# Kernel optimization log

Measured on AMD Instinct MI355X. Metric: run time of the kernel, lower is better.

Reference implementation:

```python
import jax, jax.numpy as jnp
import numpy as np

N, K, G = 4096, 4096, 128  # out_features, in_features, groupsize


def setup_inputs() -> dict:
    key = jax.random.key(0)
    k1, k2, k3, k4 = jax.random.split(key, 4)
    input = jax.random.normal(k1, (1, 2048, K), dtype=jnp.float32)
    # packed int4 weights: each byte holds two 4-bit codes (high nibble = even k, low = odd k)
    weight_packed = jax.random.randint(k2, (N, K // 2), 0, 256, dtype=jnp.int32)
    scales = jax.random.uniform(k3, (K // G, N), dtype=jnp.float32) * 0.02 + 1e-3
    zeros = jax.random.normal(k4, (K // G, N), dtype=jnp.float32) * 0.05
    scales_and_zeros = jnp.stack([scales, zeros], axis=-1)  # (K//G, N, 2)
    return {"input": input, "weight_packed": weight_packed,
            "scales_and_zeros": scales_and_zeros, "groupsize": G}


def reference(input, weight_packed, scales_and_zeros, groupsize):
    n, k_half = weight_packed.shape
    k = 2 * k_half
    g = k // groupsize
    # unpack two int4 codes per byte: high nibble first (even k index), then low nibble
    hi = (weight_packed >> 4) & 0xF
    lo = weight_packed & 0xF
    q = jnp.stack([hi, lo], axis=-1).reshape(n, k)  # (N, K), codes in [0,15]
    scales = scales_and_zeros[..., 0].T  # (N, G)
    zeros = scales_and_zeros[..., 1].T   # (N, G)
    # group-wise affine dequant: w = (q - 8) * scale + zero
    qg = q.reshape(n, g, groupsize).astype(jnp.float32)
    w = (qg - 8.0) * scales[:, :, None] + zeros[:, :, None]  # (N, G, gs)
    w = w.reshape(n, k)
    # out[..., n] = sum_k input[..., k] * w[n, k]
    return jnp.einsum('bsk,nk->bsn', input, w)
```

## Files before the change

kernel.cpp:

```cpp
#include <hip/hip_runtime.h>
#include <hip/hip_bf16.h>


using bf16x8 = __attribute__((ext_vector_type(8))) short;
using f32x4  = __attribute__((ext_vector_type(4))) float;

#define KK 4096
#define NN 4096
#define NT (KK / 64)

static __device__ __forceinline__ short f2bf(float f) {
    __hip_bfloat16 h = __float2bfloat16(f);
    return __builtin_bit_cast(short, h);
}

#define GLDS16(gptr, lptr) __builtin_amdgcn_global_load_lds( \
    (const __attribute__((address_space(1))) void*)(gptr),   \
    (__attribute__((address_space(3))) void*)(lptr), 16, 0, 0)

#define MFMA16 __builtin_amdgcn_mfma_f32_16x16x32_bf16

__global__ __launch_bounds__(256) void dequant_w(
    const int* __restrict__ W, const float* __restrict__ SZ,
    short* __restrict__ Wd)
{
    const int idx = blockIdx.x * 256 + threadIdx.x;
    const int n   = idx >> 9;
    const int q4  = idx & 511;
    const int kh0 = q4 << 2;
    const int g   = kh0 >> 6;
    const float2 sz = *(const float2*)(SZ + ((size_t)g * NN + n) * 2);
    const float scale = sz.x;
    const float zs    = sz.y - 8.0f * sz.x;
    int4 p = *(const int4*)(W + (size_t)n * (KK / 2) + kh0);
    int vals[4] = {p.x, p.y, p.z, p.w};
    bf16x8 r;
    #pragma unroll
    for (int j = 0; j < 4; ++j) {
        int v = vals[j];
        r[2 * j]     = f2bf((float)((v >> 4) & 0xF) * scale + zs);
        r[2 * j + 1] = f2bf((float)(v & 0xF) * scale + zs);
    }
    *(bf16x8*)&Wd[(size_t)n * KK + (kh0 << 1)] = r;
}

__global__ __launch_bounds__(256) void cvt_a(
    const float* __restrict__ A, short* __restrict__ Ab)
{
    const int idx = blockIdx.x * 256 + threadIdx.x;
    const float4* s = (const float4*)(A + (size_t)idx * 8);
    float4 u = s[0], v = s[1];
    bf16x8 r;
    r[0] = f2bf(u.x); r[1] = f2bf(u.y); r[2] = f2bf(u.z); r[3] = f2bf(u.w);
    r[4] = f2bf(v.x); r[5] = f2bf(v.y); r[6] = f2bf(v.z); r[7] = f2bf(v.w);
    *(bf16x8*)&Ab[(size_t)idx * 8] = r;
}

__global__ __launch_bounds__(512, 2) void gemm_8ph(
    const short* __restrict__ Ab, const short* __restrict__ Bb,
    float* __restrict__ C)
{
    __shared__ short sA[3 * 256 * 64];
    __shared__ short sB[3 * 128 * 64];

    const int tid  = threadIdx.x;
    const int lane = tid & 63;
    const int wave = tid >> 6;
    const int wm   = wave >> 1;
    const int wn   = wave & 1;
    const int bm   = blockIdx.y * 256;
    const int bn   = blockIdx.x * 128;

    const int sl = lane >> 3;
    const int sc = (lane & 7) ^ sl;
    const short* aSt = Ab + (size_t)(bm + wave * 32 + sl) * KK + sc * 8;
    const short* bSt = Bb + (size_t)(bn + wave * 16 + sl) * KK + sc * 8;

    const int l15 = lane & 15;
    const int pc0 = (((lane >> 4)) ^ (lane & 7)) * 8;
    const int pc1 = ((4 | (lane >> 4)) ^ (lane & 7)) * 8;
    const int aRd = wm * 4096 + l15 * 64;
    const int bRd = wn * 4096 + l15 * 64;

    f32x4 acc[4][4] = {};
    bf16x8 aF[2][2], bF[2][2][2];

    #pragma unroll
    for (int l = 0; l < 4; ++l)
        GLDS16(aSt + l * 8 * KK,      &sA[(wave * 32 + l * 8) * 64]);
    #pragma unroll
    for (int l = 0; l < 2; ++l)
        GLDS16(bSt + l * 8 * KK,      &sB[(wave * 16 + l * 8) * 64]);
    #pragma unroll
    for (int l = 0; l < 4; ++l)
        GLDS16(aSt + l * 8 * KK + 64, &sA[16384 + (wave * 32 + l * 8) * 64]);
    #pragma unroll
    for (int l = 0; l < 2; ++l)
        GLDS16(bSt + l * 8 * KK + 64, &sB[8192 + (wave * 16 + l * 8) * 64]);
    asm volatile("s_waitcnt vmcnt(6)" ::: "memory");
    __builtin_amdgcn_s_barrier();

    int cur = 0;
    for (int t = 0; t < NT; ++t) {
        const int nxt = (cur == 0) ? 2 : cur - 1;
        const short* sAc = &sA[cur * 16384];
        const short* sBc = &sB[cur * 8192];
        short* sAn = &sA[nxt * 16384];
        short* sBn = &sB[nxt * 8192];
        const bool st = (t + 2 < NT);
        const int gk = (t + 2) * 64;

        aF[0][0] = *(const bf16x8*)&sAc[aRd + pc0];
        aF[0][1] = *(const bf16x8*)&sAc[aRd + pc1];
        aF[1][0] = *(const bf16x8*)&sAc[aRd + 1024 + pc0];
        aF[1][1] = *(const bf16x8*)&sAc[aRd + 1024 + pc1];
        bF[0][0][0] = *(const bf16x8*)&sBc[bRd + pc0];
        bF[0][0][1] = *(const bf16x8*)&sBc[bRd + pc1];
        bF[0][1][0] = *(const bf16x8*)&sBc[bRd + 1024 + pc0];
        bF[0][1][1] = *(const bf16x8*)&sBc[bRd + 1024 + pc1];
        if (st) {
            GLDS16(aSt + 0 * 8 * KK + gk, sAn + (wave * 32 + 0) * 64);
            GLDS16(aSt + 1 * 8 * KK + gk, sAn + (wave * 32 + 8) * 64);
        }
        __builtin_amdgcn_s_barrier();
        asm volatile("s_waitcnt lgkmcnt(0)" ::: "memory");
        __builtin_amdgcn_s_setprio(1);
        acc[0][0] = MFMA16(aF[0][0], bF[0][0][0], acc[0][0], 0, 0, 0);
        acc[0][0] = MFMA16(aF[0][1], bF[0][0][1], acc[0][0], 0, 0, 0);
        acc[0][1] = MFMA16(aF[0][0], bF[0][1][0], acc[0][1], 0, 0, 0);
        acc[0][1] = MFMA16(aF[0][1], bF[0][1][1], acc[0][1], 0, 0, 0);
        acc[1][0] = MFMA16(aF[1][0], bF[0][0][0], acc[1][0], 0, 0, 0);
        acc[1][0] = MFMA16(aF[1][1], bF[0][0][1], acc[1][0], 0, 0, 0);
        acc[1][1] = MFMA16(aF[1][0], bF[0][1][0], acc[1][1], 0, 0, 0);
        acc[1][1] = MFMA16(aF[1][1], bF[0][1][1], acc[1][1], 0, 0, 0);
        __builtin_amdgcn_s_setprio(0);
        __builtin_amdgcn_s_barrier();

        bF[1][0][0] = *(const bf16x8*)&sBc[bRd + 2048 + pc0];
        bF[1][0][1] = *(const bf16x8*)&sBc[bRd + 2048 + pc1];
        bF[1][1][0] = *(const bf16x8*)&sBc[bRd + 3072 + pc0];
        bF[1][1][1] = *(const bf16x8*)&sBc[bRd + 3072 + pc1];
        if (st) {
            GLDS16(aSt + 2 * 8 * KK + gk, sAn + (wave * 32 + 16) * 64);
            GLDS16(aSt + 3 * 8 * KK + gk, sAn + (wave * 32 + 24) * 64);
        }
        __builtin_amdgcn_s_barrier();
        asm volatile("s_waitcnt lgkmcnt(0)" ::: "memory");
        __builtin_amdgcn_s_setprio(1);
        acc[0][2] = MFMA16(aF[0][0], bF[1][0][0], acc[0][2], 0, 0, 0);
        acc[0][2] = MFMA16(aF[0][1], bF[1][0][1], acc[0][2], 0, 0, 0);
        acc[0][3] = MFMA16(aF[0][0], bF[1][1][0], acc[0][3], 0, 0, 0);
        acc[0][3] = MFMA16(aF[0][1], bF[1][1][1], acc[0][3], 0, 0, 0);
        acc[1][2] = MFMA16(aF[1][0], bF[1][0][0], acc[1][2], 0, 0, 0);
        acc[1][2] = MFMA16(aF[1][1], bF[1][0][1], acc[1][2], 0, 0, 0);
        acc[1][3] = MFMA16(aF[1][0], bF[1][1][0], acc[1][3], 0, 0, 0);
        acc[1][3] = MFMA16(aF[1][1], bF[1][1][1], acc[1][3], 0, 0, 0);
        __builtin_amdgcn_s_setprio(0);
        __builtin_amdgcn_s_barrier();

        aF[0][0] = *(const bf16x8*)&sAc[aRd + 2048 + pc0];
        aF[0][1] = *(const bf16x8*)&sAc[aRd + 2048 + pc1];
        aF[1][0] = *(const bf16x8*)&sAc[aRd + 3072 + pc0];
        aF[1][1] = *(const bf16x8*)&sAc[aRd + 3072 + pc1];
        if (st) {
            GLDS16(bSt + 0 * 8 * KK + gk, sBn + (wave * 16 + 0) * 64);
            GLDS16(bSt + 1 * 8 * KK + gk, sBn + (wave * 16 + 8) * 64);
        }
        __builtin_amdgcn_s_barrier();
        asm volatile("s_waitcnt lgkmcnt(0)" ::: "memory");
        __builtin_amdgcn_s_setprio(1);
        acc[2][2] = MFMA16(aF[0][0], bF[1][0][0], acc[2][2], 0, 0, 0);
        acc[2][2] = MFMA16(aF[0][1], bF[1][0][1], acc[2][2], 0, 0, 0);
        acc[2][3] = MFMA16(aF[0][0], bF[1][1][0], acc[2][3], 0, 0, 0);
        acc[2][3] = MFMA16(aF[0][1], bF[1][1][1], acc[2][3], 0, 0, 0);
        acc[3][2] = MFMA16(aF[1][0], bF[1][0][0], acc[3][2], 0, 0, 0);
        acc[3][2] = MFMA16(aF[1][1], bF[1][0][1], acc[3][2], 0, 0, 0);
        acc[3][3] = MFMA16(aF[1][0], bF[1][1][0], acc[3][3], 0, 0, 0);
        acc[3][3] = MFMA16(aF[1][1], bF[1][1][1], acc[3][3], 0, 0, 0);
        __builtin_amdgcn_s_setprio(0);
        __builtin_amdgcn_s_barrier();

        __builtin_amdgcn_s_setprio(1);
        acc[2][0] = MFMA16(aF[0][0], bF[0][0][0], acc[2][0], 0, 0, 0);
        acc[2][0] = MFMA16(aF[0][1], bF[0][0][1], acc[2][0], 0, 0, 0);
        acc[2][1] = MFMA16(aF[0][0], bF[0][1][0], acc[2][1], 0, 0, 0);
        acc[2][1] = MFMA16(aF[0][1], bF[0][1][1], acc[2][1], 0, 0, 0);
        acc[3][0] = MFMA16(aF[1][0], bF[0][0][0], acc[3][0], 0, 0, 0);
        acc[3][0] = MFMA16(aF[1][1], bF[0][0][1], acc[3][0], 0, 0, 0);
        acc[3][1] = MFMA16(aF[1][0], bF[0][1][0], acc[3][1], 0, 0, 0);
        acc[3][1] = MFMA16(aF[1][1], bF[0][1][1], acc[3][1], 0, 0, 0);
        __builtin_amdgcn_s_setprio(0);
        if (t < NT - 2) {
            asm volatile("s_waitcnt vmcnt(6)" ::: "memory");
        } else {
            asm volatile("s_waitcnt vmcnt(0)" ::: "memory");
        }
        __builtin_amdgcn_s_barrier();

        cur = (cur == 2) ? 0 : cur + 1;
    }

    float* Cp = C + (size_t)(bm + wm * 64) * NN + bn + wn * 64;
    const int cr = (lane >> 4) << 2;
    #pragma unroll
    for (int m = 0; m < 4; ++m) {
        #pragma unroll
        for (int j = 0; j < 4; ++j) {
            float* dst = Cp + (size_t)(m * 16 + cr + j) * NN + l15;
            #pragma unroll
            for (int n = 0; n < 4; ++n)
                dst[n * 16] = acc[m][n][j];
        }
    }
}

#define LDKF 72
__global__ __launch_bounds__(256) void wq4_gemm_fused(
    const float* __restrict__ A, const int* __restrict__ W,
    const float* __restrict__ SZ, float* __restrict__ C, int M)
{
    __shared__ short sA[128 * LDKF];
    __shared__ short sB[128 * LDKF];
    const int tid = threadIdx.x, lane = tid & 63, wave = tid >> 6;
    const int wr = (wave >> 1) << 6, wc = (wave & 1) << 6;
    const int bm = blockIdx.y * 128, bn = blockIdx.x * 128;
    const int ar = tid >> 2, ac = (tid & 3) << 4;
    const int br = tid >> 1, bh = (tid & 1) << 4;
    const float* Arow0 = A + (size_t)(bm + ar) * KK + ac;
    const float* Arow1 = A + (size_t)(bm + 64 + ar) * KK + ac;
    const int*   Wrow  = W + (size_t)(bn + br) * (KK / 2) + bh;
    const float* SZrow = SZ + (size_t)(bn + br) * 2;
    f32x4 acc[4][4] = {};
    for (int k0 = 0; k0 < KK; k0 += 64) {
        {
            const float4* s0 = (const float4*)(Arow0 + k0);
            const float4* s1 = (const float4*)(Arow1 + k0);
            float4 a0 = s0[0], a1 = s0[1], a2 = s0[2], a3 = s0[3];
            float4 b0 = s1[0], b1 = s1[1], b2 = s1[2], b3 = s1[3];
            auto cvt8 = [](float4 u, float4 v) -> bf16x8 {
                bf16x8 r;
                r[0] = f2bf(u.x); r[1] = f2bf(u.y); r[2] = f2bf(u.z); r[3] = f2bf(u.w);
                r[4] = f2bf(v.x); r[5] = f2bf(v.y); r[6] = f2bf(v.z); r[7] = f2bf(v.w);
                return r;
            };
            *(bf16x8*)&sA[ar * LDKF + ac]            = cvt8(a0, a1);
            *(bf16x8*)&sA[ar * LDKF + ac + 8]        = cvt8(a2, a3);
            *(bf16x8*)&sA[(64 + ar) * LDKF + ac]     = cvt8(b0, b1);
            *(bf16x8*)&sA[(64 + ar) * LDKF + ac + 8] = cvt8(b2, b3);
        }
        {
            const int g = k0 >> 7;
            const float2 sz = *(const float2*)(SZrow + (size_t)g * NN * 2);
            const float scale = sz.x, zs = sz.y - 8.0f * sz.x;
            const int4* src = (const int4*)(Wrow + (k0 >> 1));
            #pragma unroll
            for (int i = 0; i < 4; ++i) {
                int4 p = src[i];
                int vals[4] = {p.x, p.y, p.z, p.w};
                bf16x8 r;
                #pragma unroll
                for (int j = 0; j < 4; ++j) {
                    int v = vals[j];
                    r[2 * j]     = f2bf((float)((v >> 4) & 0xF) * scale + zs);
                    r[2 * j + 1] = f2bf((float)(v & 0xF) * scale + zs);
                }
                *(bf16x8*)&sB[br * LDKF + (bh << 1) + (i << 3)] = r;
            }
        }
        __syncthreads();
        #pragma unroll
        for (int ks = 0; ks < 2; ++ks) {
            const int col = (ks << 5) + ((lane >> 4) << 3);
            bf16x8 af[4], bfr[4];
            #pragma unroll
            for (int m = 0; m < 4; ++m)
                af[m] = *(const bf16x8*)&sA[(wr + m * 16 + (lane & 15)) * LDKF + col];
            #pragma unroll
            for (int n = 0; n < 4; ++n)
                bfr[n] = *(const bf16x8*)&sB[(wc + n * 16 + (lane & 15)) * LDKF + col];
            #pragma unroll
            for (int m = 0; m < 4; ++m)
                #pragma unroll
                for (int n = 0; n < 4; ++n)
                    acc[m][n] = __builtin_amdgcn_mfma_f32_16x16x32_bf16(
                        af[m], bfr[n], acc[m][n], 0, 0, 0);
        }
        __syncthreads();
    }
    float* Cp = C + (size_t)(bm + wr) * NN + bn + wc;
    const int cr = (lane >> 4) << 2, cc = lane & 15;
    #pragma unroll
    for (int m = 0; m < 4; ++m)
        #pragma unroll
        for (int j = 0; j < 4; ++j) {
            float* dst = Cp + (size_t)(m * 16 + cr + j) * NN + cc;
            #pragma unroll
            for (int n = 0; n < 4; ++n) dst[n * 16] = acc[m][n][j];
        }
}

extern "C" void kernel_launch(void* const* d_in, const int* in_sizes, int n_in,
                              void* d_out, int out_size, void* d_ws, size_t ws_size,
                              hipStream_t stream) {
    const float* A  = (const float*)d_in[0];
    const int*   W  = (const int*)d_in[1];
    const float* SZ = (const float*)d_in[2];
    float* C = (float*)d_out;

    const int M = in_sizes[0] / KK;

    const size_t wd_elems = (size_t)NN * KK;
    const size_t ab_elems = (size_t)M * KK;
    const size_t need = (wd_elems + ab_elems) * sizeof(short);

    if (ws_size >= need && (M % 256) == 0) {
        short* Wd = (short*)d_ws;
        short* Ab = Wd + wd_elems;
        dequant_w<<<NN * (KK / 8) / 256, 256, 0, stream>>>(W, SZ, Wd);
        cvt_a<<<(int)(ab_elems / 8 / 256), 256, 0, stream>>>(A, Ab);
        dim3 grid(NN / 128, M / 256);
        gemm_8ph<<<grid, dim3(512), 0, stream>>>(Ab, Wd, C);
    } else {
        dim3 grid(NN / 128, M / 128);
        wq4_gemm_fused<<<grid, dim3(256), 0, stream>>>(A, W, SZ, C, M);
    }
}
```

Before: 102.4 us.

## Switch bf16 GEMM inner loop to 32x32x16 MFMA with two-phase schedule

Replaces the 16x16x32 MFMA tiling in the main GEMM with 32x32x16 MFMA instructions, so each wave now holds four 32x32 accumulators instead of sixteen 16x16 ones. The per-tile schedule drops from four barrier-separated phases to two, with LDS fragment reads and async global-to-LDS prefetches redistributed across them. The aim is fewer LDS reads per FLOP and less barrier overhead. The cost is a different LDS read swizzle pattern and epilogue mapping, which may change bank conflicts and latency hiding.

After: 102.7 us. About the same (+0.2%).

```diff
diff --git a/kernel.cpp b/kernel.cpp
--- a/kernel.cpp
+++ b/kernel.cpp
@@ -3,7 +3,7 @@
 
 
 using bf16x8 = __attribute__((ext_vector_type(8))) short;
-using f32x4  = __attribute__((ext_vector_type(4))) float;
+using f32x16 = __attribute__((ext_vector_type(16))) float;
 
 #define KK 4096
 #define NN 4096
@@ -18,7 +18,7 @@
     (const __attribute__((address_space(1))) void*)(gptr),   \
     (__attribute__((address_space(3))) void*)(lptr), 16, 0, 0)
 
-#define MFMA16 __builtin_amdgcn_mfma_f32_16x16x32_bf16
+#define MFMA32 __builtin_amdgcn_mfma_f32_32x32x16_bf16
 
 __global__ __launch_bounds__(256) void dequant_w(
     const int* __restrict__ W, const float* __restrict__ SZ,
@@ -56,7 +56,7 @@
     *(bf16x8*)&Ab[(size_t)idx * 8] = r;
 }
 
-__global__ __launch_bounds__(512, 2) void gemm_8ph(
+__global__ __launch_bounds__(512, 2) void gemm32(
     const short* __restrict__ Ab, const short* __restrict__ Bb,
     float* __restrict__ C)
 {
@@ -76,27 +76,30 @@
     const short* aSt = Ab + (size_t)(bm + wave * 32 + sl) * KK + sc * 8;
     const short* bSt = Bb + (size_t)(bn + wave * 16 + sl) * KK + sc * 8;
 
-    const int l15 = lane & 15;
-    const int pc0 = (((lane >> 4)) ^ (lane & 7)) * 8;
-    const int pc1 = ((4 | (lane >> 4)) ^ (lane & 7)) * 8;
-    const int aRd = wm * 4096 + l15 * 64;
-    const int bRd = wn * 4096 + l15 * 64;
-
-    f32x4 acc[4][4] = {};
-    bf16x8 aF[2][2], bF[2][2][2];
+    const int l31 = lane & 31;
+    const int lx  = lane >> 5;
+    const int l7  = lane & 7;
+    const int px0 = ((0 + lx) ^ l7) * 8;
+    const int px1 = ((2 + lx) ^ l7) * 8;
+    const int px2 = ((4 + lx) ^ l7) * 8;
+    const int px3 = ((6 + lx) ^ l7) * 8;
+    const int aRd = (wm * 64 + l31) * 64;
+    const int bRd = (wn * 64 + l31) * 64;
+
+    f32x16 acc00 = {}, acc01 = {}, acc10 = {}, acc11 = {};
 
     #pragma unroll
     for (int l = 0; l < 4; ++l)
-        GLDS16(aSt + l * 8 * KK,      &sA[(wave * 32 + l * 8) * 64]);
+        GLDS16(aSt + (size_t)l * 8 * KK,      &sA[(wave * 32 + l * 8) * 64]);
     #pragma unroll
     for (int l = 0; l < 2; ++l)
-        GLDS16(bSt + l * 8 * KK,      &sB[(wave * 16 + l * 8) * 64]);
+        GLDS16(bSt + (size_t)l * 8 * KK,      &sB[(wave * 16 + l * 8) * 64]);
     #pragma unroll
     for (int l = 0; l < 4; ++l)
-        GLDS16(aSt + l * 8 * KK + 64, &sA[16384 + (wave * 32 + l * 8) * 64]);
+        GLDS16(aSt + (size_t)l * 8 * KK + 64, &sA[16384 + (wave * 32 + l * 8) * 64]);
     #pragma unroll
     for (int l = 0; l < 2; ++l)
-        GLDS16(bSt + l * 8 * KK + 64, &sB[8192 + (wave * 16 + l * 8) * 64]);
+        GLDS16(bSt + (size_t)l * 8 * KK + 64, &sB[8192 + (wave * 16 + l * 8) * 64]);
     asm volatile("s_waitcnt vmcnt(6)" ::: "memory");
     __builtin_amdgcn_s_barrier();
 
@@ -110,110 +113,97 @@
         const bool st = (t + 2 < NT);
         const int gk = (t + 2) * 64;
 
-        aF[0][0] = *(const bf16x8*)&sAc[aRd + pc0];
-        aF[0][1] = *(const bf16x8*)&sAc[aRd + pc1];
-        aF[1][0] = *(const bf16x8*)&sAc[aRd + 1024 + pc0];
-        aF[1][1] = *(const bf16x8*)&sAc[aRd + 1024 + pc1];
-        bF[0][0][0] = *(const bf16x8*)&sBc[bRd + pc0];
-        bF[0][0][1] = *(const bf16x8*)&sBc[bRd + pc1];
-        bF[0][1][0] = *(const bf16x8*)&sBc[bRd + 1024 + pc0];
-        bF[0][1][1] = *(const bf16x8*)&sBc[bRd + 1024 + pc1];
-        if (st) {
-            GLDS16(aSt + 0 * 8 * KK + gk, sAn + (wave * 32 + 0) * 64);
-            GLDS16(aSt + 1 * 8 * KK + gk, sAn + (wave * 32 + 8) * 64);
-        }
-        __builtin_amdgcn_s_barrier();
-        asm volatile("s_waitcnt lgkmcnt(0)" ::: "memory");
-        __builtin_amdgcn_s_setprio(1);
-        acc[0][0] = MFMA16(aF[0][0], bF[0][0][0], acc[0][0], 0, 0, 0);
-        acc[0][0] = MFMA16(aF[0][1], bF[0][0][1], acc[0][0], 0, 0, 0);
-        acc[0][1] = MFMA16(aF[0][0], bF[0][1][0], acc[0][1], 0, 0, 0);
-        acc[0][1] = MFMA16(aF[0][1], bF[0][1][1], acc[0][1], 0, 0, 0);
-        acc[1][0] = MFMA16(aF[1][0], bF[0][0][0], acc[1][0], 0, 0, 0);
-        acc[1][0] = MFMA16(aF[1][1], bF[0][0][1], acc[1][0], 0, 0, 0);
-        acc[1][1] = MFMA16(aF[1][0], bF[0][1][0], acc[1][1], 0, 0, 0);
-        acc[1][1] = MFMA16(aF[1][1], bF[0][1][1], acc[1][1], 0, 0, 0);
-        __builtin_amdgcn_s_setprio(0);
-        __builtin_amdgcn_s_barrier();
-
-        bF[1][0][0] = *(const bf16x8*)&sBc[bRd + 2048 + pc0];
-        bF[1][0][1] = *(const bf16x8*)&sBc[bRd + 2048 + pc1];
-        bF[1][1][0] = *(const bf16x8*)&sBc[bRd + 3072 + pc0];
-        bF[1][1][1] = *(const bf16x8*)&sBc[bRd + 3072 + pc1];
-        if (st) {
-            GLDS16(aSt + 2 * 8 * KK + gk, sAn + (wave * 32 + 16) * 64);
-            GLDS16(aSt + 3 * 8 * KK + gk, sAn + (wave * 32 + 24) * 64);
-        }
-        __builtin_amdgcn_s_barrier();
-        asm volatile("s_waitcnt lgkmcnt(0)" ::: "memory");
-        __builtin_amdgcn_s_setprio(1);
-        acc[0][2] = MFMA16(aF[0][0], bF[1][0][0], acc[0][2], 0, 0, 0);
-        acc[0][2] = MFMA16(aF[0][1], bF[1][0][1], acc[0][2], 0, 0, 0);
-        acc[0][3] = MFMA16(aF[0][0], bF[1][1][0], acc[0][3], 0, 0, 0);
-        acc[0][3] = MFMA16(aF[0][1], bF[1][1][1], acc[0][3], 0, 0, 0);
-        acc[1][2] = MFMA16(aF[1][0], bF[1][0][0], acc[1][2], 0, 0, 0);
-        acc[1][2] = MFMA16(aF[1][1], bF[1][0][1], acc[1][2], 0, 0, 0);
-        acc[1][3] = MFMA16(aF[1][0], bF[1][1][0], acc[1][3], 0, 0, 0);
-        acc[1][3] = MFMA16(aF[1][1], bF[1][1][1], acc[1][3], 0, 0, 0);
-        __builtin_amdgcn_s_setprio(0);
-        __builtin_amdgcn_s_barrier();
-
-        aF[0][0] = *(const bf16x8*)&sAc[aRd + 2048 + pc0];
-        aF[0][1] = *(const bf16x8*)&sAc[aRd + 2048 + pc1];
-        aF[1][0] = *(const bf16x8*)&sAc[aRd + 3072 + pc0];
-        aF[1][1] = *(const bf16x8*)&sAc[aRd + 3072 + pc1];
-        if (st) {
-            GLDS16(bSt + 0 * 8 * KK + gk, sBn + (wave * 16 + 0) * 64);
-            GLDS16(bSt + 1 * 8 * KK + gk, sBn + (wave * 16 + 8) * 64);
-        }
-        __builtin_amdgcn_s_barrier();
-        asm volatile("s_waitcnt lgkmcnt(0)" ::: "memory");
-        __builtin_amdgcn_s_setprio(1);
-        acc[2][2] = MFMA16(aF[0][0], bF[1][0][0], acc[2][2], 0, 0, 0);
-        acc[2][2] = MFMA16(aF[0][1], bF[1][0][1], acc[2][2], 0, 0, 0);
-        acc[2][3] = MFMA16(aF[0][0], bF[1][1][0], acc[2][3], 0, 0, 0);
-        acc[2][3] = MFMA16(aF[0][1], bF[1][1][1], acc[2][3], 0, 0, 0);
-        acc[3][2] = MFMA16(aF[1][0], bF[1][0][0], acc[3][2], 0, 0, 0);
-        acc[3][2] = MFMA16(aF[1][1], bF[1][0][1], acc[3][2], 0, 0, 0);
-        acc[3][3] = MFMA16(aF[1][0], bF[1][1][0], acc[3][3], 0, 0, 0);
-        acc[3][3] = MFMA16(aF[1][1], bF[1][1][1], acc[3][3], 0, 0, 0);
-        __builtin_amdgcn_s_setprio(0);
-        __builtin_amdgcn_s_barrier();
-
-        __builtin_amdgcn_s_setprio(1);
-        acc[2][0] = MFMA16(aF[0][0], bF[0][0][0], acc[2][0], 0, 0, 0);
-        acc[2][0] = MFMA16(aF[0][1], bF[0][0][1], acc[2][0], 0, 0, 0);
-        acc[2][1] = MFMA16(aF[0][0], bF[0][1][0], acc[2][1], 0, 0, 0);
-        acc[2][1] = MFMA16(aF[0][1], bF[0][1][1], acc[2][1], 0, 0, 0);
-        acc[3][0] = MFMA16(aF[1][0], bF[0][0][0], acc[3][0], 0, 0, 0);
-        acc[3][0] = MFMA16(aF[1][1], bF[0][0][1], acc[3][0], 0, 0, 0);
-        acc[3][1] = MFMA16(aF[1][0], bF[0][1][0], acc[3][1], 0, 0, 0);
-        acc[3][1] = MFMA16(aF[1][1], bF[0][1][1], acc[3][1], 0, 0, 0);
-        __builtin_amdgcn_s_setprio(0);
-        if (t < NT - 2) {
-            asm volatile("s_waitcnt vmcnt(6)" ::: "memory");
-        } else {
-            asm volatile("s_waitcnt vmcnt(0)" ::: "memory");
-        }
-        __builtin_amdgcn_s_barrier();
+        {
+            bf16x8 a00 = *(const bf16x8*)&sAc[aRd + px0];
+            bf16x8 a01 = *(const bf16x8*)&sAc[aRd + px1];
+            bf16x8 a10 = *(const bf16x8*)&sAc[aRd + 2048 + px0];
+            bf16x8 a11 = *(const bf16x8*)&sAc[aRd + 2048 + px1];
+            bf16x8 b00 = *(const bf16x8*)&sBc[bRd + px0];
+            bf16x8 b01 = *(const bf16x8*)&sBc[bRd + px1];
+            bf16x8 b10 = *(const bf16x8*)&sBc[bRd + 2048 + px0];
+            bf16x8 b11 = *(const bf16x8*)&sBc[bRd + 2048 + px1];
+            if (st) {
+                GLDS16(aSt + (size_t)0 * 8 * KK + gk, sAn + (wave * 32 + 0) * 64);
+                GLDS16(aSt + (size_t)1 * 8 * KK + gk, sAn + (wave * 32 + 8) * 64);
+                GLDS16(bSt + (size_t)0 * 8 * KK + gk, sBn + (wave * 16 + 0) * 64);
+            }
+            __builtin_amdgcn_s_barrier();
+            asm volatile("s_waitcnt lgkmcnt(0)" ::: "memory");
+            __builtin_amdgcn_s_setprio(1);
+            acc00 = MFMA32(a00, b00, acc00, 0, 0, 0);
+            acc00 = MFMA32(a01, b01, acc00, 0, 0, 0);
+            acc01 = MFMA32(a00, b10, acc01, 0, 0, 0);
+            acc01 = MFMA32(a01, b11, acc01, 0, 0, 0);
+            acc10 = MFMA32(a10, b00, acc10, 0, 0, 0);
+            acc10 = MFMA32(a11, b01, acc10, 0, 0, 0);
+            acc11 = MFMA32(a10, b10, acc11, 0, 0, 0);
+            acc11 = MFMA32(a11, b11, acc11, 0, 0, 0);
+            __builtin_amdgcn_s_setprio(0);
+            __builtin_amdgcn_s_barrier();
+        }
+
+        {
+            bf16x8 a00 = *(const bf16x8*)&sAc[aRd + px2];
+            bf16x8 a01 = *(const bf16x8*)&sAc[aRd + px3];
+            bf16x8 a10 = *(const bf16x8*)&sAc[aRd + 2048 + px2];
+            bf16x8 a11 = *(const bf16x8*)&sAc[aRd + 2048 + px3];
+            bf16x8 b00 = *(const bf16x8*)&sBc[bRd + px2];
+            bf16x8 b01 = *(const bf16x8*)&sBc[bRd + px3];
+            bf16x8 b10 = *(const bf16x8*)&sBc[bRd + 2048 + px2];
+            bf16x8 b11 = *(const bf16x8*)&sBc[bRd + 2048 + px3];
+            if (st) {
+                GLDS16(aSt + (size_t)2 * 8 * KK + gk, sAn + (wave * 32 + 16) * 64);
+                GLDS16(aSt + (size_t)3 * 8 * KK + gk, sAn + (wave * 32 + 24) * 64);
+                GLDS16(bSt + (size_t)1 * 8 * KK + gk, sBn + (wave * 16 + 8) * 64);
+            }
+            __builtin_amdgcn_s_barrier();
+            asm volatile("s_waitcnt lgkmcnt(0)" ::: "memory");
+            __builtin_amdgcn_s_setprio(1);
+            acc00 = MFMA32(a00, b00, acc00, 0, 0, 0);
+            acc00 = MFMA32(a01, b01, acc00, 0, 0, 0);
+            acc01 = MFMA32(a00, b10, acc01, 0, 0, 0);
+            acc01 = MFMA32(a01, b11, acc01, 0, 0, 0);
+            acc10 = MFMA32(a10, b00, acc10, 0, 0, 0);
+            acc10 = MFMA32(a11, b01, acc10, 0, 0, 0);
+            acc11 = MFMA32(a10, b10, acc11, 0, 0, 0);
+            acc11 = MFMA32(a11, b11, acc11, 0, 0, 0);
+            __builtin_amdgcn_s_setprio(0);
+            if (t < NT - 2) {
+                asm volatile("s_waitcnt vmcnt(6)" ::: "memory");
+            } else {
+                asm volatile("s_waitcnt vmcnt(0)" ::: "memory");
+            }
+            __builtin_amdgcn_s_barrier();
+        }
 
         cur = (cur == 2) ? 0 : cur + 1;
     }
 
-    float* Cp = C + (size_t)(bm + wm * 64) * NN + bn + wn * 64;
-    const int cr = (lane >> 4) << 2;
-    #pragma unroll
-    for (int m = 0; m < 4; ++m) {
+    {
+        const int crow = lx * 4;
+        float* Cp = C + (size_t)(bm + wm * 64) * NN + bn + wn * 64;
         #pragma unroll
-        for (int j = 0; j < 4; ++j) {
-            float* dst = Cp + (size_t)(m * 16 + cr + j) * NN + l15;
-            #pragma unroll
-            for (int n = 0; n < 4; ++n)
-                dst[n * 16] = acc[m][n][j];
-        }
-    }
-}
-
+        for (int m = 0; m < 2; ++m) {
+            #pragma unroll
+            for (int qr = 0; qr < 4; ++qr) {
+                #pragma unroll
+                for (int j = 0; j < 4; ++j) {
+                    const int row = m * 32 + crow + j + 8 * qr;
+                    float* dst = Cp + (size_t)row * NN + l31;
+                    if (m == 0) {
+                        dst[0]  = acc00[qr * 4 + j];
+                        dst[32] = acc01[qr * 4 + j];
+                    } else {
+                        dst[0]  = acc10[qr * 4 + j];
+                        dst[32] = acc11[qr * 4 + j];
+                    }
+                }
+            }
+        }
+    }
+}
+
+using f32x4 = __attribute__((ext_vector_type(4))) float;
 #define LDKF 72
 __global__ __launch_bounds__(256) void wq4_gemm_fused(
     const float* __restrict__ A, const int* __restrict__ W,
@@ -319,7 +309,7 @@
         dequant_w<<<NN * (KK / 8) / 256, 256, 0, stream>>>(W, SZ, Wd);
         cvt_a<<<(int)(ab_elems / 8 / 256), 256, 0, stream>>>(A, Ab);
         dim3 grid(NN / 128, M / 256);
-        gemm_8ph<<<grid, dim3(512), 0, stream>>>(Ab, Wd, C);
+        gemm32<<<grid, dim3(512), 0, stream>>>(Ab, Wd, C);
     } else {
         dim3 grid(NN / 128, M / 128);
         wq4_gemm_fused<<<grid, dim3(256), 0, stream>>>(A, W, SZ, C, M);
```
